# Kernel tuning notes

Measured on AMD Instinct MI355X. Metric: run time of the kernel, lower is better.

The kernel has to match this reference:

```python
import jax, jax.numpy as jnp
import numpy as np

B, T, D = 2, 2048, 1024
DCD = 4096            # intermediate_dim
RET = 128             # expert_retrieval_dim (split into 2 halves of 64)
NEXP = 4096           # num experts (perfect square)
NKEYS = 64            # sqrt(NEXP)
H = 4                 # n_experts_heads
KPH = 8               # n_experts_per_head


def setup_inputs() -> dict:
    key = jax.random.key(0)
    ks = jax.random.split(key, 10)
    s = lambda k, shape, scale: jax.random.normal(k, shape, jnp.float32) * scale
    return {
        "hidden_states": jax.random.normal(ks[0], (B, T, D), jnp.float32),
        "Wg": s(ks[1], (D, DCD), 0.02), "bg": jnp.zeros((DCD,), jnp.float32),
        "Wu": s(ks[2], (D, DCD), 0.02), "bu": jnp.zeros((DCD,), jnp.float32),
        "Wd": s(ks[3], (DCD, D), 0.02), "bd": jnp.zeros((D,), jnp.float32),
        "Wq": s(ks[4], (D, RET * H), 0.02),          # queries proj (no bias)
        "keys": s(ks[5], (H, NKEYS, 2, RET // 2), 0.02),  # torch inits zeros; randn for a meaningful baseline
        "down_embed": s(ks[6], (NEXP, D), 0.02),
        "up_embed": s(ks[7], (NEXP, D), 0.02),
    }


def reference(hidden_states, Wg, bg, Wu, bu, Wd, bd, Wq, keys, down_embed, up_embed):
    b, t, d = hidden_states.shape
    # product-key retrieval: split query into two halves (p=2)
    q = (hidden_states @ Wq).reshape(b, t, 2, H, RET // 2)
    sim = jnp.einsum('btphn,hkpn->pbthk', q, keys)          # [2,b,t,H,NKEYS]
    sc, ix = jax.lax.top_k(sim, KPH)                        # per-half top-k
    sx, sy = sc[0], sc[1]
    ixx, ixy = ix[0], ix[1]
    all_sc = (sx[..., :, None] + sy[..., None, :]).reshape(b, t, H, KPH * KPH)
    all_ix = (ixx[..., :, None] * NKEYS + ixy[..., None, :]).reshape(b, t, H, KPH * KPH)
    scores, pk = jax.lax.top_k(all_sc, KPH)                 # [b,t,H,KPH]
    idx = jnp.take_along_axis(all_ix, pk, axis=-1)          # expert ids
    de = down_embed[idx]                                    # [b,t,H,KPH,D] gather
    ue = up_embed[idx]                                      # [b,t,H,KPH,D] gather
    w = jnp.einsum('btd,bthkd->bthk', hidden_states, de)
    w = jax.nn.silu(w) * jax.nn.softmax(scores, axis=-1)
    experts_states = jnp.einsum('bthk,bthkd->btd', w, ue)
    mlp = (jax.nn.silu(hidden_states @ Wg + bg) * (hidden_states @ Wu + bu)) @ Wd + bd
    return mlp + experts_states
```

## Files before the change

### kernel.cpp

```cpp
#include <hip/hip_runtime.h>
#include <hip/hip_bf16.h>
#include <stdint.h>

typedef unsigned short u16;
typedef __attribute__((ext_vector_type(8))) short short8;
typedef __attribute__((ext_vector_type(4))) float f32x4;

union B8 { short8 v; u16 u[8]; };
union U4 { unsigned long long q; u16 u[4]; };

__device__ __forceinline__ float b2f(u16 b) {
  union { unsigned int i; float f; } x; x.i = ((unsigned int)b) << 16; return x.f;
}
__device__ __forceinline__ u16 f2b(float f) {
  __hip_bfloat16 h = __float2bfloat16(f);
  return *reinterpret_cast<u16*>(&h);
}

#define GLOAD_LDS16(gp, lp)                                                  \
  __builtin_amdgcn_global_load_lds(                                          \
      (const __attribute__((address_space(1))) unsigned int*)(gp),           \
      (__attribute__((address_space(3))) unsigned int*)(lp), 16, 0, 0)

__global__ __launch_bounds__(256) void cvt_f2b(const float* __restrict__ src,
                                               u16* __restrict__ dst) {
  size_t i = ((size_t)blockIdx.x * 256 + threadIdx.x) * 4;
  f32x4 v = *(const f32x4*)(src + i);
  U4 o;
#pragma unroll
  for (int j = 0; j < 4; ++j) o.u[j] = f2b(v[j]);
  *(unsigned long long*)(dst + i) = o.q;
}

__global__ __launch_bounds__(256) void convt_w(const float* __restrict__ W,
                                               u16* __restrict__ WT,
                                               int K, int N) {
  int k  = blockIdx.x * 64 + (threadIdx.x & 63);
  int n8 = blockIdx.y * 32 + (threadIdx.x >> 6) * 8;
  const float* p = W + (size_t)k * N + n8;
  f32x4 a = *(const f32x4*)(p);
  f32x4 b = *(const f32x4*)(p + 4);
#pragma unroll
  for (int j = 0; j < 4; ++j) WT[(size_t)(n8 + j) * K + k] = f2b(a[j]);
#pragma unroll
  for (int j = 0; j < 4; ++j) WT[(size_t)(n8 + 4 + j) * K + k] = f2b(b[j]);
}

__global__ __launch_bounds__(256) void gemm_bf16(
    const u16* __restrict__ A, const u16* __restrict__ BT,
    const float* __restrict__ bias,
    u16* __restrict__ Cb, int M, int N, int K)
{
  __shared__ __attribute__((aligned(16))) u16 As[128 * 32];
  __shared__ __attribute__((aligned(16))) u16 Bs[128 * 32];
  int tid = threadIdx.x;
  int m0 = blockIdx.y * 128, n0 = blockIdx.x * 128;
  int wave = tid >> 6, lane = tid & 63;
  int wm = (wave >> 1) * 64, wn = (wave & 1) * 64;
  int quad = lane >> 4, r16 = lane & 15;
  int seg0 = wave * 2, seg1 = wave * 2 + 1;
  int srow = lane >> 2, scol = (lane & 3) * 8;

  const u16* a0 = A  + (size_t)(m0 + seg0 * 16 + srow) * K + scol;
  const u16* a1 = A  + (size_t)(m0 + seg1 * 16 + srow) * K + scol;
  const u16* b0 = BT + (size_t)(n0 + seg0 * 16 + srow) * K + scol;
  const u16* b1 = BT + (size_t)(n0 + seg1 * 16 + srow) * K + scol;

  f32x4 acc[4][4] = {};

  for (int k0 = 0; k0 < K; k0 += 32) {
    GLOAD_LDS16(a0 + k0, As + seg0 * 512);
    GLOAD_LDS16(a1 + k0, As + seg1 * 512);
    GLOAD_LDS16(b0 + k0, Bs + seg0 * 512);
    GLOAD_LDS16(b1 + k0, Bs + seg1 * 512);
    __syncthreads();
    short8 af[4], bfr[4];
#pragma unroll
    for (int i = 0; i < 4; ++i)
      af[i] = *(const short8*)(&As[(wm + i * 16 + r16) * 32 + quad * 8]);
#pragma unroll
    for (int j = 0; j < 4; ++j)
      bfr[j] = *(const short8*)(&Bs[(wn + j * 16 + r16) * 32 + quad * 8]);
#pragma unroll
    for (int i = 0; i < 4; ++i)
#pragma unroll
      for (int j = 0; j < 4; ++j)
        acc[i][j] = __builtin_amdgcn_mfma_f32_16x16x32_bf16(af[i], bfr[j], acc[i][j], 0, 0, 0);
    __syncthreads();
  }

#pragma unroll
  for (int i = 0; i < 4; ++i) {
    int row = m0 + wm + i * 16 + quad * 4;
#pragma unroll
    for (int j = 0; j < 4; ++j) {
      int col = n0 + wn + j * 16 + r16;
      float bv = bias ? bias[col] : 0.f;
#pragma unroll
      for (int r = 0; r < 4; ++r) {
        float v = acc[i][j][r] + bv;
        Cb[(size_t)(row + r) * N + col] = f2b(v);
      }
    }
  }
}

__global__ __launch_bounds__(256) void gemm_dsk(
    const u16* __restrict__ A, const u16* __restrict__ BT,
    float* __restrict__ P, int M, int N, int K, int Kslice, int mOff)
{
  __shared__ __attribute__((aligned(16))) u16 As[128 * 32];
  __shared__ __attribute__((aligned(16))) u16 Bs[128 * 32];
  int tid = threadIdx.x;
  int m0 = blockIdx.y * 128, n0 = blockIdx.x * 128;
  int kb = blockIdx.z * Kslice, ke = kb + Kslice;
  int wave = tid >> 6, lane = tid & 63;
  int wm = (wave >> 1) * 64, wn = (wave & 1) * 64;
  int quad = lane >> 4, r16 = lane & 15;
  int seg0 = wave * 2, seg1 = wave * 2 + 1;
  int srow = lane >> 2, scol = (lane & 3) * 8;

  const u16* a0 = A  + (size_t)(m0 + seg0 * 16 + srow) * K + scol;
  const u16* a1 = A  + (size_t)(m0 + seg1 * 16 + srow) * K + scol;
  const u16* b0 = BT + (size_t)(n0 + seg0 * 16 + srow) * K + scol;
  const u16* b1 = BT + (size_t)(n0 + seg1 * 16 + srow) * K + scol;

  f32x4 acc[4][4] = {};

  for (int k0 = kb; k0 < ke; k0 += 32) {
    GLOAD_LDS16(a0 + k0, As + seg0 * 512);
    GLOAD_LDS16(a1 + k0, As + seg1 * 512);
    GLOAD_LDS16(b0 + k0, Bs + seg0 * 512);
    GLOAD_LDS16(b1 + k0, Bs + seg1 * 512);
    __syncthreads();
    short8 af[4], bfr[4];
#pragma unroll
    for (int i = 0; i < 4; ++i)
      af[i] = *(const short8*)(&As[(wm + i * 16 + r16) * 32 + quad * 8]);
#pragma unroll
    for (int j = 0; j < 4; ++j)
      bfr[j] = *(const short8*)(&Bs[(wn + j * 16 + r16) * 32 + quad * 8]);
#pragma unroll
    for (int i = 0; i < 4; ++i)
#pragma unroll
      for (int j = 0; j < 4; ++j)
        acc[i][j] = __builtin_amdgcn_mfma_f32_16x16x32_bf16(af[i], bfr[j], acc[i][j], 0, 0, 0);
    __syncthreads();
  }

  float* Pz = P + (size_t)blockIdx.z * 4194304;
#pragma unroll
  for (int i = 0; i < 4; ++i) {
    int row = mOff + m0 + wm + i * 16 + quad * 4;
#pragma unroll
    for (int j = 0; j < 4; ++j) {
      int col = n0 + wn + j * 16 + r16;
#pragma unroll
      for (int r = 0; r < 4; ++r)
        Pz[(size_t)(row + r) * N + col] = acc[i][j][r];
    }
  }
}

__global__ __launch_bounds__(256) void reduce_k(const float* __restrict__ part,
                                                int S,
                                                const float* __restrict__ es,
                                                const float* __restrict__ bd,
                                                float* __restrict__ out) {
  int t = blockIdx.x, c0 = threadIdx.x * 4;
  size_t off = (size_t)t * 1024 + c0;
  f32x4 a = *(const f32x4*)(es + off);
  for (int s = 0; s < S; ++s) {
    f32x4 p = *(const f32x4*)(part + (size_t)s * 4194304 + off);
#pragma unroll
    for (int c = 0; c < 4; ++c) a[c] += p[c];
  }
  f32x4 b = *(const f32x4*)(bd + c0);
  f32x4 o;
#pragma unroll
  for (int c = 0; c < 4; ++c) o[c] = a[c] + b[c];
  *(f32x4*)(out + off) = o;
}

__global__ __launch_bounds__(256, 2) void gemm_gu(
    const u16* __restrict__ A, const u16* __restrict__ BgT,
    const u16* __restrict__ BuT,
    const float* __restrict__ bg, const float* __restrict__ bu,
    u16* __restrict__ H, int M, int N, int K)
{
  __shared__ __attribute__((aligned(16))) u16 As[128 * 32];
  __shared__ __attribute__((aligned(16))) u16 Gs[128 * 32];
  __shared__ __attribute__((aligned(16))) u16 Us[128 * 32];
  int tid = threadIdx.x;
  int m0 = blockIdx.y * 128, n0 = blockIdx.x * 128;
  int wave = tid >> 6, lane = tid & 63;
  int wm = (wave >> 1) * 64, wn = (wave & 1) * 64;
  int quad = lane >> 4, r16 = lane & 15;
  int seg0 = wave * 2, seg1 = wave * 2 + 1;
  int srow = lane >> 2, scol = (lane & 3) * 8;

  const u16* a0 = A   + (size_t)(m0 + seg0 * 16 + srow) * K + scol;
  const u16* a1 = A   + (size_t)(m0 + seg1 * 16 + srow) * K + scol;
  const u16* g0 = BgT + (size_t)(n0 + seg0 * 16 + srow) * K + scol;
  const u16* g1 = BgT + (size_t)(n0 + seg1 * 16 + srow) * K + scol;
  const u16* u0 = BuT + (size_t)(n0 + seg0 * 16 + srow) * K + scol;
  const u16* u1 = BuT + (size_t)(n0 + seg1 * 16 + srow) * K + scol;

  f32x4 ag[4][4] = {}, au[4][4] = {};

  for (int k0 = 0; k0 < K; k0 += 32) {
    GLOAD_LDS16(a0 + k0, As + seg0 * 512);
    GLOAD_LDS16(a1 + k0, As + seg1 * 512);
    GLOAD_LDS16(g0 + k0, Gs + seg0 * 512);
    GLOAD_LDS16(g1 + k0, Gs + seg1 * 512);
    GLOAD_LDS16(u0 + k0, Us + seg0 * 512);
    GLOAD_LDS16(u1 + k0, Us + seg1 * 512);
    __syncthreads();
    short8 af[4], bfr[4];
#pragma unroll
    for (int i = 0; i < 4; ++i)
      af[i] = *(const short8*)(&As[(wm + i * 16 + r16) * 32 + quad * 8]);
#pragma unroll
    for (int j = 0; j < 4; ++j)
      bfr[j] = *(const short8*)(&Gs[(wn + j * 16 + r16) * 32 + quad * 8]);
#pragma unroll
    for (int i = 0; i < 4; ++i)
#pragma unroll
      for (int j = 0; j < 4; ++j)
        ag[i][j] = __builtin_amdgcn_mfma_f32_16x16x32_bf16(af[i], bfr[j], ag[i][j], 0, 0, 0);
#pragma unroll
    for (int j = 0; j < 4; ++j)
      bfr[j] = *(const short8*)(&Us[(wn + j * 16 + r16) * 32 + quad * 8]);
#pragma unroll
    for (int i = 0; i < 4; ++i)
#pragma unroll
      for (int j = 0; j < 4; ++j)
        au[i][j] = __builtin_amdgcn_mfma_f32_16x16x32_bf16(af[i], bfr[j], au[i][j], 0, 0, 0);
    __syncthreads();
  }

#pragma unroll
  for (int i = 0; i < 4; ++i) {
    int row = m0 + wm + i * 16 + quad * 4;
#pragma unroll
    for (int j = 0; j < 4; ++j) {
      int col = n0 + wn + j * 16 + r16;
      float bgv = bg[col], buv = bu[col];
#pragma unroll
      for (int r = 0; r < 4; ++r) {
        float g = ag[i][j][r] + bgv;
        float u = au[i][j][r] + buv;
        float h = (g / (1.f + __expf(-g))) * u;
        H[(size_t)(row + r) * N + col] = f2b(h);
      }
    }
  }
}

template<int NP>
__device__ __forceinline__ void sort8_desc(float (&v)[NP], int (&ii)[NP], int j) {
#pragma unroll
  for (int k = 2; k <= 8; k <<= 1) {
#pragma unroll
    for (int s = k >> 1; s > 0; s >>= 1) {
      bool desc  = (j & k) == 0;
      bool lower = (j & s) == 0;
#pragma unroll
      for (int p = 0; p < NP; ++p) {
        float vp = __shfl_xor(v[p], s);
        int   ip = __shfl_xor(ii[p], s);
        bool mf = (v[p] > vp) || (v[p] == vp && ii[p] < ip);
        bool keep = (desc == lower) ? mf : !mf;
        if (!keep) { v[p] = vp; ii[p] = ip; }
      }
    }
  }
}

template<int NP>
__device__ __forceinline__ void merge_top8(float (&v)[NP], int (&ii)[NP], int j) {
#pragma unroll
  for (int r = 0; r < 3; ++r) {
    int mask = (8 << r) | 7;
#pragma unroll
    for (int p = 0; p < NP; ++p) {
      float vp = __shfl_xor(v[p], mask);
      int   ip = __shfl_xor(ii[p], mask);
      bool mf = (v[p] > vp) || (v[p] == vp && ii[p] < ip);
      if (!mf) { v[p] = vp; ii[p] = ip; }
    }
#pragma unroll
    for (int s = 4; s > 0; s >>= 1) {
      bool lower = (j & s) == 0;
#pragma unroll
      for (int p = 0; p < NP; ++p) {
        float vq = __shfl_xor(v[p], s);
        int   iq = __shfl_xor(ii[p], s);
        bool mf = (v[p] > vq) || (v[p] == vq && ii[p] < iq);
        bool keep = lower ? mf : !mf;
        if (!keep) { v[p] = vq; ii[p] = iq; }
      }
    }
  }
}

__global__ __launch_bounds__(256) void retrieve_k(
    const u16*  __restrict__ q,
    const float* __restrict__ keys,
    int* __restrict__ idx_out,
    float* __restrict__ p_out)
{
  int t = blockIdx.x;
  int w = threadIdx.x >> 6, lane = threadIdx.x & 63;
  int j = lane & 7;

  float v[2]; int ii[2];
#pragma unroll
  for (int p = 0; p < 2; ++p) {
    const u16*   qp = q + (size_t)t * 512 + p * 256 + w * 64;
    const float* kp = keys + (size_t)((w * 64 + lane) * 2 + p) * 64;
    float s = 0.f;
#pragma unroll
    for (int n = 0; n < 64; n += 8) {
      B8 qv; qv.v = *(const short8*)(qp + n);
      f32x4 k0 = *(const f32x4*)(kp + n);
      f32x4 k1 = *(const f32x4*)(kp + n + 4);
#pragma unroll
      for (int c = 0; c < 4; ++c) s += b2f(qv.u[c]) * k0[c];
#pragma unroll
      for (int c = 0; c < 4; ++c) s += b2f(qv.u[4 + c]) * k1[c];
    }
    v[p] = s; ii[p] = lane;
  }

  sort8_desc<2>(v, ii, j);
  merge_top8<2>(v, ii, j);

  float v2[1] = { __shfl(v[0], lane >> 3) + __shfl(v[1], lane & 7) };
  int  pos[1] = { lane };
  merge_top8<1>(v2, pos, j);

  int ex = __shfl(ii[0], pos[0] >> 3);
  int ey = __shfl(ii[1], pos[0] & 7);

  float m = __shfl(v2[0], 0);
  float e = __expf(v2[0] - m);
  float sum = e;
#pragma unroll
  for (int s = 4; s > 0; s >>= 1) sum += __shfl_xor(sum, s);

  if (lane < 8) {
    int o = (t * 4 + w) * 8 + lane;
    p_out[o]   = e / sum;
    idx_out[o] = ex * 64 + ey;
  }
}

__global__ __launch_bounds__(256) void expert_k(
    const u16* __restrict__ xb, const u16* __restrict__ downb,
    const u16* __restrict__ upb,
    const int* __restrict__ idx, const float* __restrict__ probs,
    float* __restrict__ es)
{
  __shared__ float acc_s[4][1024];
  int t = blockIdx.x;
  int w = threadIdx.x >> 6, lane = threadIdx.x & 63;
  const size_t tb = (size_t)t * 1024;
  const int lo = lane * 8;

  B8 xv0, xv1;
  xv0.v = *(const short8*)(xb + tb + lo);
  xv1.v = *(const short8*)(xb + tb + 512 + lo);
  float xf[16];
#pragma unroll
  for (int c = 0; c < 8; ++c) { xf[c] = b2f(xv0.u[c]); xf[8 + c] = b2f(xv1.u[c]); }

  float a[16] = {};
#pragma unroll
  for (int e8 = 0; e8 < 8; ++e8) {
    int e = w * 8 + e8;
    int id = idx[t * 32 + e];
    const u16* dp = downb + (size_t)id * 1024;
    B8 d0, d1;
    d0.v = *(const short8*)(dp + lo);
    d1.v = *(const short8*)(dp + 512 + lo);
    float part = 0.f;
#pragma unroll
    for (int c = 0; c < 8; ++c)
      part += xf[c] * b2f(d0.u[c]) + xf[8 + c] * b2f(d1.u[c]);
#pragma unroll
    for (int off = 32; off; off >>= 1) part += __shfl_xor(part, off);
    float gate = (part / (1.f + __expf(-part))) * probs[t * 32 + e];
    const u16* upp = upb + (size_t)id * 1024;
    B8 u0, u1;
    u0.v = *(const short8*)(upp + lo);
    u1.v = *(const short8*)(upp + 512 + lo);
#pragma unroll
    for (int c = 0; c < 8; ++c) {
      a[c]     += gate * b2f(u0.u[c]);
      a[8 + c] += gate * b2f(u1.u[c]);
    }
  }
#pragma unroll
  for (int c = 0; c < 8; ++c) {
    acc_s[w][lo + c]       = a[c];
    acc_s[w][512 + lo + c] = a[8 + c];
  }
  __syncthreads();
  int d0i = threadIdx.x * 4;
  f32x4 s0 = *(const f32x4*)(&acc_s[0][d0i]);
  f32x4 s1 = *(const f32x4*)(&acc_s[1][d0i]);
  f32x4 s2 = *(const f32x4*)(&acc_s[2][d0i]);
  f32x4 s3 = *(const f32x4*)(&acc_s[3][d0i]);
  f32x4 o;
#pragma unroll
  for (int c = 0; c < 4; ++c) o[c] = (s0[c] + s1[c]) + (s2[c] + s3[c]);
  *(f32x4*)(es + tb + d0i) = o;
}

extern "C" void kernel_launch(void* const* d_in, const int* in_sizes, int n_in,
                              void* d_out, int out_size, void* d_ws, size_t ws_size,
                              hipStream_t stream)
{
  const float* x    = (const float*)d_in[0];
  const float* Wg   = (const float*)d_in[1];
  const float* bg   = (const float*)d_in[2];
  const float* Wu   = (const float*)d_in[3];
  const float* bu   = (const float*)d_in[4];
  const float* Wd   = (const float*)d_in[5];
  const float* bd   = (const float*)d_in[6];
  const float* Wq   = (const float*)d_in[7];
  const float* keys = (const float*)d_in[8];
  const float* down = (const float*)d_in[9];
  const float* up   = (const float*)d_in[10];
  float* out = (float*)d_out;

  const size_t MB = 1048576;
  char* ws = (char*)d_ws;
  u16*   xb    = (u16*)(ws);
  u16*   WgT   = (u16*)(ws + 8  * MB);
  u16*   WuT   = (u16*)(ws + 16 * MB);
  u16*   WdT   = (u16*)(ws + 24 * MB);
  float* es    = (float*)(ws + 32 * MB);
  u16*   WqT   = (u16*)(ws + 32 * MB);
  u16*   qb    = (u16*)(ws + 34 * MB);
  int*   idxb  = (int*)(ws + 48 * MB);
  float* prb   = (float*)(ws + 48 * MB + 512 * 1024);
  u16*   downb = (u16*)(ws + 49 * MB);
  u16*   upb   = (u16*)(ws + 57 * MB);

  int S = 4;
  while (S > 1 && 65 * MB + (size_t)S * 16 * MB + 1 * MB > ws_size) S >>= 1;
  float* part = (float*)(ws + 65 * MB);
  size_t gboff = 65 * MB + (size_t)S * 16 * MB;
  u16*   gb    = (u16*)(ws + gboff);

  size_t avail = ws_size > gboff ? ws_size - gboff : 0;
  int rows = 4096;
  while (rows > 128 && (size_t)rows * 4096 * 2 > avail) rows >>= 1;
  int Ksl = 4096 / S;

  cvt_f2b<<<4096, 256, 0, stream>>>(x, xb);
  cvt_f2b<<<4096, 256, 0, stream>>>(down, downb);
  cvt_f2b<<<4096, 256, 0, stream>>>(up, upb);
  convt_w<<<dim3(16, 16),  256, 0, stream>>>(Wq, WqT, 1024, 512);
  convt_w<<<dim3(16, 128), 256, 0, stream>>>(Wg, WgT, 1024, 4096);
  convt_w<<<dim3(16, 128), 256, 0, stream>>>(Wu, WuT, 1024, 4096);
  convt_w<<<dim3(64, 32),  256, 0, stream>>>(Wd, WdT, 4096, 1024);

  gemm_bf16<<<dim3(4, 32), 256, 0, stream>>>(xb, WqT, nullptr,
                                             qb, 4096, 512, 1024);
  retrieve_k<<<4096, 256, 0, stream>>>(qb, keys, idxb, prb);
  expert_k<<<4096, 256, 0, stream>>>(xb, downb, upb, idxb, prb, es);

  for (int m0c = 0; m0c < 4096; m0c += rows) {
    int gy = rows / 128;
    gemm_gu<<<dim3(32, gy), 256, 0, stream>>>(xb + (size_t)m0c * 1024, WgT, WuT,
                                              bg, bu, gb, rows, 4096, 1024);
    gemm_dsk<<<dim3(8, gy, S), 256, 0, stream>>>(gb, WdT, part,
                                                 rows, 1024, 4096, Ksl, m0c);
  }
  reduce_k<<<4096, 256, 0, stream>>>(part, S, es, bd, out);
}
```

Measured before the change: 488.0 us.

## Replace MLP GEMMs with triple-buffered 256x128 swizzled-LDS GEMM kernel

Replaces the fused gate/up GEMM and the split-K down GEMM with one templated-by-mode 512-thread kernel. It uses 256x128 tiles, a BK=64 triple-buffered LDS pipeline with explicit vmcnt waits, XOR-swizzled LDS layout and raised MFMA priority. Gate and up are now computed as two separate launches, with the up result stored as bf16 in workspace and read back in the gate epilogue. Split-K for the down projection is fixed at 2 and the row-chunking workspace fallback is removed. The aim is better MFMA utilization and latency hiding, at the cost of an extra intermediate buffer round trip, an extra bf16 rounding of the up projection, and larger fixed workspace needs.

```diff
diff --git a/kernel.cpp b/kernel.cpp
--- a/kernel.cpp
+++ b/kernel.cpp
@@ -105,59 +105,108 @@
   }
 }
 
-__global__ __launch_bounds__(256) void gemm_dsk(
+__global__ __launch_bounds__(512, 2) void g8(
     const u16* __restrict__ A, const u16* __restrict__ BT,
-    float* __restrict__ P, int M, int N, int K, int Kslice, int mOff)
+    const float* __restrict__ bias, const u16* __restrict__ U,
+    void* __restrict__ out, int N, int K, int Kslice, int mode)
 {
-  __shared__ __attribute__((aligned(16))) u16 As[128 * 32];
-  __shared__ __attribute__((aligned(16))) u16 Bs[128 * 32];
+  __shared__ __attribute__((aligned(16))) u16 lds[73728];
   int tid = threadIdx.x;
-  int m0 = blockIdx.y * 128, n0 = blockIdx.x * 128;
-  int kb = blockIdx.z * Kslice, ke = kb + Kslice;
-  int wave = tid >> 6, lane = tid & 63;
-  int wm = (wave >> 1) * 64, wn = (wave & 1) * 64;
-  int quad = lane >> 4, r16 = lane & 15;
-  int seg0 = wave * 2, seg1 = wave * 2 + 1;
-  int srow = lane >> 2, scol = (lane & 3) * 8;
-
-  const u16* a0 = A  + (size_t)(m0 + seg0 * 16 + srow) * K + scol;
-  const u16* a1 = A  + (size_t)(m0 + seg1 * 16 + srow) * K + scol;
-  const u16* b0 = BT + (size_t)(n0 + seg0 * 16 + srow) * K + scol;
-  const u16* b1 = BT + (size_t)(n0 + seg1 * 16 + srow) * K + scol;
+  int m0 = blockIdx.y * 256, n0 = blockIdx.x * 128;
+  int kb = blockIdx.z * Kslice;
+  int wid = tid >> 6, l = tid & 63;
+  int waveM = wid & 3, waveN = wid >> 2;
+  int quad = l >> 4, r16 = l & 15;
+  int NT = Kslice >> 6;
+
+  size_t soff = (size_t)(l >> 3) * K + (size_t)(((l & 7) ^ (l >> 3)) << 3);
+  const u16* Ag = A  + (size_t)(m0 + wid * 8) * K + kb + soff;
+  const u16* Bg = BT + (size_t)(n0 + wid * 8) * K + kb + soff;
 
   f32x4 acc[4][4] = {};
-
-  for (int k0 = kb; k0 < ke; k0 += 32) {
-    GLOAD_LDS16(a0 + k0, As + seg0 * 512);
-    GLOAD_LDS16(a1 + k0, As + seg1 * 512);
-    GLOAD_LDS16(b0 + k0, Bs + seg0 * 512);
-    GLOAD_LDS16(b1 + k0, Bs + seg1 * 512);
-    __syncthreads();
-    short8 af[4], bfr[4];
-#pragma unroll
-    for (int i = 0; i < 4; ++i)
-      af[i] = *(const short8*)(&As[(wm + i * 16 + r16) * 32 + quad * 8]);
-#pragma unroll
-    for (int j = 0; j < 4; ++j)
-      bfr[j] = *(const short8*)(&Bs[(wn + j * 16 + r16) * 32 + quad * 8]);
-#pragma unroll
-    for (int i = 0; i < 4; ++i)
-#pragma unroll
-      for (int j = 0; j < 4; ++j)
-        acc[i][j] = __builtin_amdgcn_mfma_f32_16x16x32_bf16(af[i], bfr[j], acc[i][j], 0, 0, 0);
-    __syncthreads();
-  }
-
-  float* Pz = P + (size_t)blockIdx.z * 4194304;
-#pragma unroll
-  for (int i = 0; i < 4; ++i) {
-    int row = mOff + m0 + wm + i * 16 + quad * 4;
-#pragma unroll
-    for (int j = 0; j < 4; ++j) {
-      int col = n0 + wn + j * 16 + r16;
-#pragma unroll
-      for (int r = 0; r < 4; ++r)
-        Pz[(size_t)(row + r) * N + col] = acc[i][j][r];
+  int arow = (waveM * 64 + r16) * 64;
+  int brow = (waveN * 64 + r16) * 64;
+  int s7 = r16 & 7;
+
+#define STAGE_A(t, c) GLOAD_LDS16(Ag + (size_t)(c) * 64 * K + (size_t)(t) * 64, \
+                                  lds + ((t) % 3) * 24576 + (c) * 4096 + wid * 512)
+#define STAGE_B(t, c) GLOAD_LDS16(Bg + (size_t)(c) * 64 * K + (size_t)(t) * 64, \
+                                  lds + ((t) % 3) * 24576 + 16384 + (c) * 4096 + wid * 512)
+
+  STAGE_A(0, 0); STAGE_A(0, 1); STAGE_A(0, 2); STAGE_A(0, 3);
+  STAGE_B(0, 0); STAGE_B(0, 1);
+  STAGE_A(1, 0); STAGE_A(1, 1); STAGE_A(1, 2); STAGE_A(1, 3);
+  STAGE_B(1, 0); STAGE_B(1, 1);
+
+  for (int t = 0; t < NT; ++t) {
+    const u16* La = lds + (t % 3) * 24576;
+    const u16* Lb = La + 16384;
+    if (t + 1 < NT) asm volatile("s_waitcnt vmcnt(6)" ::: "memory");
+    else            asm volatile("s_waitcnt vmcnt(0)" ::: "memory");
+    __builtin_amdgcn_s_barrier();
+    asm volatile("" ::: "memory");
+    bool pf = (t + 2 < NT);
+#pragma unroll
+    for (int kk = 0; kk < 2; ++kk) {
+      short8 af[4], bf[4];
+#pragma unroll
+      for (int m = 0; m < 4; ++m)
+        af[m] = *(const short8*)(La + arow + m * 1024 + (((kk << 2) + quad) ^ s7) * 8);
+#pragma unroll
+      for (int n = 0; n < 4; ++n)
+        bf[n] = *(const short8*)(Lb + brow + n * 1024 + (((kk << 2) + quad) ^ s7) * 8);
+      if (pf) {
+        if (kk == 0) { STAGE_A(t + 2, 0); STAGE_A(t + 2, 1); STAGE_A(t + 2, 2); }
+        else         { STAGE_A(t + 2, 3); STAGE_B(t + 2, 0); STAGE_B(t + 2, 1); }
+      }
+      asm volatile("" ::: "memory");
+      __builtin_amdgcn_s_barrier();
+      __builtin_amdgcn_s_setprio(1);
+#pragma unroll
+      for (int m = 0; m < 4; ++m)
+#pragma unroll
+        for (int n = 0; n < 4; ++n)
+          acc[m][n] = __builtin_amdgcn_mfma_f32_16x16x32_bf16(af[m], bf[n], acc[m][n], 0, 0, 0);
+      __builtin_amdgcn_s_setprio(0);
+      if (kk == 0) { asm volatile("" ::: "memory"); __builtin_amdgcn_s_barrier(); }
+    }
+  }
+#undef STAGE_A
+#undef STAGE_B
+
+  int rbase = m0 + waveM * 64 + quad * 4;
+  int cbase = n0 + waveN * 64 + r16;
+  if (mode == 2) {
+    float* P = (float*)out + (size_t)blockIdx.z * 4194304;
+#pragma unroll
+    for (int m = 0; m < 4; ++m)
+#pragma unroll
+      for (int n = 0; n < 4; ++n)
+#pragma unroll
+        for (int r = 0; r < 4; ++r)
+          P[(size_t)(rbase + m * 16 + r) * N + cbase + n * 16] = acc[m][n][r];
+  } else {
+    u16* C = (u16*)out;
+#pragma unroll
+    for (int n = 0; n < 4; ++n) {
+      int col = cbase + n * 16;
+      float bv = bias[col];
+#pragma unroll
+      for (int m = 0; m < 4; ++m) {
+#pragma unroll
+        for (int r = 0; r < 4; ++r) {
+          int row = rbase + m * 16 + r;
+          float g = acc[m][n][r] + bv;
+          float h;
+          if (mode == 1) {
+            float u = b2f(U[(size_t)row * N + col]);
+            h = (g / (1.f + __expf(-g))) * u;
+          } else {
+            h = g;
+          }
+          C[(size_t)row * N + col] = f2b(h);
+        }
+      }
     }
   }
 }
@@ -180,81 +229,6 @@
 #pragma unroll
   for (int c = 0; c < 4; ++c) o[c] = a[c] + b[c];
   *(f32x4*)(out + off) = o;
-}
-
-__global__ __launch_bounds__(256, 2) void gemm_gu(
-    const u16* __restrict__ A, const u16* __restrict__ BgT,
-    const u16* __restrict__ BuT,
-    const float* __restrict__ bg, const float* __restrict__ bu,
-    u16* __restrict__ H, int M, int N, int K)
-{
-  __shared__ __attribute__((aligned(16))) u16 As[128 * 32];
-  __shared__ __attribute__((aligned(16))) u16 Gs[128 * 32];
-  __shared__ __attribute__((aligned(16))) u16 Us[128 * 32];
-  int tid = threadIdx.x;
-  int m0 = blockIdx.y * 128, n0 = blockIdx.x * 128;
-  int wave = tid >> 6, lane = tid & 63;
-  int wm = (wave >> 1) * 64, wn = (wave & 1) * 64;
-  int quad = lane >> 4, r16 = lane & 15;
-  int seg0 = wave * 2, seg1 = wave * 2 + 1;
-  int srow = lane >> 2, scol = (lane & 3) * 8;
-
-  const u16* a0 = A   + (size_t)(m0 + seg0 * 16 + srow) * K + scol;
-  const u16* a1 = A   + (size_t)(m0 + seg1 * 16 + srow) * K + scol;
-  const u16* g0 = BgT + (size_t)(n0 + seg0 * 16 + srow) * K + scol;
-  const u16* g1 = BgT + (size_t)(n0 + seg1 * 16 + srow) * K + scol;
-  const u16* u0 = BuT + (size_t)(n0 + seg0 * 16 + srow) * K + scol;
-  const u16* u1 = BuT + (size_t)(n0 + seg1 * 16 + srow) * K + scol;
-
-  f32x4 ag[4][4] = {}, au[4][4] = {};
-
-  for (int k0 = 0; k0 < K; k0 += 32) {
-    GLOAD_LDS16(a0 + k0, As + seg0 * 512);
-    GLOAD_LDS16(a1 + k0, As + seg1 * 512);
-    GLOAD_LDS16(g0 + k0, Gs + seg0 * 512);
-    GLOAD_LDS16(g1 + k0, Gs + seg1 * 512);
-    GLOAD_LDS16(u0 + k0, Us + seg0 * 512);
-    GLOAD_LDS16(u1 + k0, Us + seg1 * 512);
-    __syncthreads();
-    short8 af[4], bfr[4];
-#pragma unroll
-    for (int i = 0; i < 4; ++i)
-      af[i] = *(const short8*)(&As[(wm + i * 16 + r16) * 32 + quad * 8]);
-#pragma unroll
-    for (int j = 0; j < 4; ++j)
-      bfr[j] = *(const short8*)(&Gs[(wn + j * 16 + r16) * 32 + quad * 8]);
-#pragma unroll
-    for (int i = 0; i < 4; ++i)
-#pragma unroll
-      for (int j = 0; j < 4; ++j)
-        ag[i][j] = __builtin_amdgcn_mfma_f32_16x16x32_bf16(af[i], bfr[j], ag[i][j], 0, 0, 0);
-#pragma unroll
-    for (int j = 0; j < 4; ++j)
-      bfr[j] = *(const short8*)(&Us[(wn + j * 16 + r16) * 32 + quad * 8]);
-#pragma unroll
-    for (int i = 0; i < 4; ++i)
-#pragma unroll
-      for (int j = 0; j < 4; ++j)
-        au[i][j] = __builtin_amdgcn_mfma_f32_16x16x32_bf16(af[i], bfr[j], au[i][j], 0, 0, 0);
-    __syncthreads();
-  }
-
-#pragma unroll
-  for (int i = 0; i < 4; ++i) {
-    int row = m0 + wm + i * 16 + quad * 4;
-#pragma unroll
-    for (int j = 0; j < 4; ++j) {
-      int col = n0 + wn + j * 16 + r16;
-      float bgv = bg[col], buv = bu[col];
-#pragma unroll
-      for (int r = 0; r < 4; ++r) {
-        float g = ag[i][j][r] + bgv;
-        float u = au[i][j][r] + buv;
-        float h = (g / (1.f + __expf(-g))) * u;
-        H[(size_t)(row + r) * N + col] = f2b(h);
-      }
-    }
-  }
 }
 
 template<int NP>
@@ -448,17 +422,10 @@
   float* prb   = (float*)(ws + 48 * MB + 512 * 1024);
   u16*   downb = (u16*)(ws + 49 * MB);
   u16*   upb   = (u16*)(ws + 57 * MB);
-
-  int S = 4;
-  while (S > 1 && 65 * MB + (size_t)S * 16 * MB + 1 * MB > ws_size) S >>= 1;
-  float* part = (float*)(ws + 65 * MB);
-  size_t gboff = 65 * MB + (size_t)S * 16 * MB;
-  u16*   gb    = (u16*)(ws + gboff);
-
-  size_t avail = ws_size > gboff ? ws_size - gboff : 0;
-  int rows = 4096;
-  while (rows > 128 && (size_t)rows * 4096 * 2 > avail) rows >>= 1;
-  int Ksl = 4096 / S;
+  float* part  = (float*)(ws + 65 * MB);
+  u16*   Ub    = (u16*)(ws + 97 * MB);
+  u16*   gb    = (u16*)(ws + 129 * MB);
+  const int S = 2;
 
   cvt_f2b<<<4096, 256, 0, stream>>>(x, xb);
   cvt_f2b<<<4096, 256, 0, stream>>>(down, downb);
@@ -473,12 +440,11 @@
   retrieve_k<<<4096, 256, 0, stream>>>(qb, keys, idxb, prb);
   expert_k<<<4096, 256, 0, stream>>>(xb, downb, upb, idxb, prb, es);
 
-  for (int m0c = 0; m0c < 4096; m0c += rows) {
-    int gy = rows / 128;
-    gemm_gu<<<dim3(32, gy), 256, 0, stream>>>(xb + (size_t)m0c * 1024, WgT, WuT,
-                                              bg, bu, gb, rows, 4096, 1024);
-    gemm_dsk<<<dim3(8, gy, S), 256, 0, stream>>>(gb, WdT, part,
-                                                 rows, 1024, 4096, Ksl, m0c);
-  }
+  g8<<<dim3(32, 16, 1), 512, 0, stream>>>(xb, WuT, bu, nullptr, Ub,
+                                          4096, 1024, 1024, 0);
+  g8<<<dim3(32, 16, 1), 512, 0, stream>>>(xb, WgT, bg, Ub, gb,
+                                          4096, 1024, 1024, 1);
+  g8<<<dim3(8, 16, S),  512, 0, stream>>>(gb, WdT, nullptr, nullptr, part,
+                                          1024, 4096, 4096 / S, 2);
   reduce_k<<<4096, 256, 0, stream>>>(part, S, es, bd, out);
 }
```

Measured after the change: 503.6 us. 3.2% more time.
